# Performance work log

Measured on AMD Instinct MI355X. Metric: run time of the kernel, lower is better.

The kernel has to match this reference:

```python
import jax, jax.numpy as jnp
import numpy as np

DIM = 384
WIN = 16
NUM_HEADS = 12
HEAD_DIM = DIM // NUM_HEADS
SCALE = HEAD_DIM ** -0.5
EPS_NORM = 1e-12  # torch F.normalize eps


def setup_inputs() -> dict:
    key = jax.random.key(0)
    ks = jax.random.split(key, 5)
    B_ = 256
    x = jax.random.normal(ks[0], (B_, DIM, WIN, WIN), dtype=jnp.float32)
    qkv_w = jax.random.normal(ks[1], (3 * DIM, DIM), dtype=jnp.float32) * (DIM ** -0.5)
    qkv_b = jax.random.normal(ks[2], (3 * DIM,), dtype=jnp.float32) * 0.02
    proj_w = jax.random.normal(ks[3], (DIM, DIM), dtype=jnp.float32) * (DIM ** -0.5)
    proj_b = jax.random.normal(ks[4], (DIM,), dtype=jnp.float32) * 0.02
    return {"x": x, "qkv_w": qkv_w, "qkv_b": qkv_b, "proj_w": proj_w, "proj_b": proj_b}


def _l2norm(t):
    n = jnp.sqrt(jnp.sum(t * t, axis=-1, keepdims=True))
    return t / jnp.maximum(n, EPS_NORM)


def reference(x, qkv_w, qkv_b, proj_w, proj_b):
    B_, C, H, W = x.shape
    N = H * W
    xt = x.reshape(B_, C, N).transpose(0, 2, 1)  # (B_, N, C)
    qkv = jnp.einsum('bnc,oc->bno', xt, qkv_w) + qkv_b  # (B_, N, 3C)
    qkv = qkv.reshape(B_, N, 3, NUM_HEADS, HEAD_DIM).transpose(2, 0, 3, 1, 4)
    q, k, v = qkv[0], qkv[1], qkv[2]  # (B_, h, N, d)
    q = _l2norm(q)
    k = _l2norm(k)
    attn = jnp.einsum('bhnd,bhmd->bhnm', q, k) * SCALE
    attn = attn - jnp.max(attn, axis=-1, keepdims=True)
    attn = jax.nn.softmax(attn, axis=-1)
    attn = jnp.clip(attn, 1e-06, 1.0)
    out = jnp.einsum('bhnm,bhmd->bhnd', attn, v)  # (B_, h, N, d)
    out = out.transpose(0, 2, 1, 3).reshape(B_, N, C)
    out = jnp.einsum('bnc,oc->bno', out, proj_w) + proj_b
    return out.transpose(0, 2, 1).reshape(B_, C, H, W)
```

## Files before the change

### kernel.cpp

```cpp
#include <hip/hip_runtime.h>


#define DIM 384
#define NT 256
#define NH 12
#define HD 32
#define QSCALE (0.17677669529663687f * 1.4426950408889634f)

typedef __bf16 bf16;
typedef __bf16 bf16x4 __attribute__((ext_vector_type(4)));
typedef __bf16 bf16x8 __attribute__((ext_vector_type(8)));
typedef float f32x4 __attribute__((ext_vector_type(4)));
typedef int i32x2 __attribute__((ext_vector_type(2)));
typedef int i32x4 __attribute__((ext_vector_type(4)));

#define MFMA16(a, b, c) __builtin_amdgcn_mfma_f32_16x16x32_bf16(a, b, c, 0, 0, 0)

static __device__ __forceinline__ bf16x8 pack2(bf16x4 lo, bf16x4 hi) {
    i32x2 a = __builtin_bit_cast(i32x2, lo);
    i32x2 c = __builtin_bit_cast(i32x2, hi);
    i32x4 v = {a[0], a[1], c[0], c[1]};
    return __builtin_bit_cast(bf16x8, v);
}

__global__ void k_cast_w(const float* __restrict__ qkv_w, const float* __restrict__ proj_w,
                         bf16* __restrict__ wq, bf16* __restrict__ wp) {
    int i = blockIdx.x * 256 + threadIdx.x;
    if (i < 3 * DIM * DIM) wq[i] = (bf16)qkv_w[i];
    if (i < DIM * DIM)     wp[i] = (bf16)proj_w[i];
}

__global__ void k_transpose_cast(const float* __restrict__ x, bf16* __restrict__ xt) {
    __shared__ float tile[32][33];
    int b = blockIdx.z;
    int c0 = blockIdx.y * 32;
    int n0 = blockIdx.x * 32;
    int tx = threadIdx.x, ty = threadIdx.y;
    const float* xp = x + (size_t)b * DIM * NT;
#pragma unroll
    for (int i = 0; i < 4; ++i) {
        int c = c0 + ty + i * 8;
        tile[ty + i * 8][tx] = xp[(size_t)c * NT + n0 + tx];
    }
    __syncthreads();
    bf16* op = xt + (size_t)b * NT * DIM;
#pragma unroll
    for (int i = 0; i < 4; ++i) {
        int n = n0 + ty + i * 8;
        op[(size_t)n * DIM + c0 + tx] = (bf16)tile[tx][ty + i * 8];
    }
}

__launch_bounds__(512, 3)
__global__ void k_qkv_attn(const bf16* __restrict__ xt, const bf16* __restrict__ wq,
                           const float* __restrict__ qkv_b, bf16* __restrict__ attn_out) {
    __shared__ __align__(16) char smem[76800];
    bf16 (*wsm)[400] = (bf16(*)[400])smem;
    bf16 (*kn)[40]   = (bf16(*)[40])smem;
    bf16 (*vT)[264]  = (bf16(*)[264])(smem + 20480);
    bf16 (*qn)[32]   = (bf16(*)[32])(smem + 37376);
    __shared__ float bias_s[96];

    const int n_ = blockIdx.x;
    const int xcd = n_ & 7;
    const int ww = n_ >> 3;
    const int b = xcd * 32 + ww / 12;
    const int h = ww % 12;

    const int tid = threadIdx.x;
    const int lane = tid & 63, w = tid >> 6;
    const int l15 = lane & 15, quad = lane >> 4;

    if (tid < 96) {
        int which = tid >> 5;
        bias_s[tid] = qkv_b[which * DIM + h * HD + (tid & 31)];
    }
#pragma unroll
    for (int i = 0; i < 9; ++i) {
        int c = tid + i * 512;
        int row = c / 48, ch = c % 48;
        int grow = (row >> 5) * DIM + h * HD + (row & 31);
        *(bf16x8*)&wsm[row][ch * 8] = *(const bf16x8*)(wq + (size_t)grow * DIM + ch * 8);
    }
    __syncthreads();

    f32x4 acc[6][2];
#pragma unroll
    for (int jt = 0; jt < 6; ++jt)
#pragma unroll
        for (int tt = 0; tt < 2; ++tt) acc[jt][tt] = (f32x4){0.f, 0.f, 0.f, 0.f};

    const bf16* xrow[2];
#pragma unroll
    for (int tt = 0; tt < 2; ++tt) {
        int tok = w * 32 + tt * 16 + l15;
        xrow[tt] = xt + (size_t)(b * NT + tok) * DIM + quad * 8;
    }

    bf16x8 bx[2][2];
#pragma unroll
    for (int tt = 0; tt < 2; ++tt) bx[0][tt] = *(const bf16x8*)(xrow[tt]);

#pragma unroll
    for (int kc = 0; kc < 12; ++kc) {
        const int cur = kc & 1, nxt = cur ^ 1;
        if (kc < 11) {
            int k0 = (kc + 1) * 32;
#pragma unroll
            for (int tt = 0; tt < 2; ++tt) bx[nxt][tt] = *(const bf16x8*)(xrow[tt] + k0);
        }
        bf16x8 aw[6];
#pragma unroll
        for (int jt = 0; jt < 6; ++jt)
            aw[jt] = *(const bf16x8*)&wsm[jt * 16 + l15][kc * 32 + quad * 8];
#pragma unroll
        for (int jt = 0; jt < 6; ++jt)
#pragma unroll
            for (int tt = 0; tt < 2; ++tt)
                acc[jt][tt] = MFMA16(aw[jt], bx[cur][tt], acc[jt][tt]);
    }
    __syncthreads();

#pragma unroll
    for (int tt = 0; tt < 2; ++tt) {
        int tok = w * 32 + tt * 16 + l15;
        float sq = 0.f, sk = 0.f;
#pragma unroll
        for (int jt = 0; jt < 6; ++jt)
#pragma unroll
            for (int r = 0; r < 4; ++r) {
                int j = jt * 16 + quad * 4 + r;
                float t = acc[jt][tt][r] + bias_s[j];
                acc[jt][tt][r] = t;
                if (jt < 2) sq += t * t;
                else if (jt < 4) sk += t * t;
            }
        sq += __shfl_xor(sq, 16); sq += __shfl_xor(sq, 32);
        sk += __shfl_xor(sk, 16); sk += __shfl_xor(sk, 32);
        float iq = QSCALE / fmaxf(sqrtf(sq), 1e-12f);
        float ik = 1.f / fmaxf(sqrtf(sk), 1e-12f);

        bf16x4 q0v, q1v, k0v, k1v;
#pragma unroll
        for (int r = 0; r < 4; ++r) {
            q0v[r] = (bf16)(acc[0][tt][r] * iq);
            q1v[r] = (bf16)(acc[1][tt][r] * iq);
            k0v[r] = (bf16)(acc[2][tt][r] * ik);
            k1v[r] = (bf16)(acc[3][tt][r] * ik);
        }
        *(bf16x4*)&qn[tok][quad * 4]      = q0v;
        *(bf16x4*)&qn[tok][16 + quad * 4] = q1v;
        *(bf16x4*)&kn[tok][quad * 4]      = k0v;
        *(bf16x4*)&kn[tok][16 + quad * 4] = k1v;
#pragma unroll
        for (int r = 0; r < 4; ++r) {
            vT[quad * 4 + r][tok]      = (bf16)acc[4][tt][r];
            vT[16 + quad * 4 + r][tok] = (bf16)acc[5][tt][r];
        }
    }
    __syncthreads();

    bf16x8 qa[2];
#pragma unroll
    for (int qt = 0; qt < 2; ++qt)
        qa[qt] = *(const bf16x8*)&qn[w * 32 + qt * 16 + l15][quad * 8];

    const f32x4 zf = {0.f, 0.f, 0.f, 0.f};
    f32x4 o[2][2];
#pragma unroll
    for (int qt = 0; qt < 2; ++qt) { o[qt][0] = zf; o[qt][1] = zf; }
    float dsm[2] = {0.f, 0.f};

    bf16x8 kb0 = *(const bf16x8*)&kn[l15][quad * 8];
    bf16x8 kb1 = *(const bf16x8*)&kn[16 + l15][quad * 8];
    bf16x4 vp0 = *(const bf16x4*)&vT[l15][quad * 4];
    bf16x4 vp1 = *(const bf16x4*)&vT[l15][16 + quad * 4];
    bf16x4 vp2 = *(const bf16x4*)&vT[16 + l15][quad * 4];
    bf16x4 vp3 = *(const bf16x4*)&vT[16 + l15][16 + quad * 4];

#pragma unroll
    for (int kt = 0; kt < 8; ++kt) {
        f32x4 s00 = MFMA16(kb0, qa[0], zf);
        f32x4 s01 = MFMA16(kb1, qa[0], zf);
        f32x4 s10 = MFMA16(kb0, qa[1], zf);
        f32x4 s11 = MFMA16(kb1, qa[1], zf);
        bf16x8 vb0 = pack2(vp0, vp1);
        bf16x8 vb1 = pack2(vp2, vp3);
        if (kt < 7) {
            int nk = kt * 32 + 32;
            kb0 = *(const bf16x8*)&kn[nk + l15][quad * 8];
            kb1 = *(const bf16x8*)&kn[nk + 16 + l15][quad * 8];
            vp0 = *(const bf16x4*)&vT[l15][nk + quad * 4];
            vp1 = *(const bf16x4*)&vT[l15][nk + 16 + quad * 4];
            vp2 = *(const bf16x4*)&vT[16 + l15][nk + quad * 4];
            vp3 = *(const bf16x4*)&vT[16 + l15][nk + 16 + quad * 4];
        }
        bf16x8 pa0, pa1;
        float d0 = 0.f, d1 = 0.f;
#pragma unroll
        for (int r = 0; r < 4; ++r) {
            float p00 = __builtin_amdgcn_exp2f(s00[r]);
            float p01 = __builtin_amdgcn_exp2f(s01[r]);
            float p10 = __builtin_amdgcn_exp2f(s10[r]);
            float p11 = __builtin_amdgcn_exp2f(s11[r]);
            d0 += p00 + p01;  d1 += p10 + p11;
            pa0[r] = (bf16)p00; pa0[4 + r] = (bf16)p01;
            pa1[r] = (bf16)p10; pa1[4 + r] = (bf16)p11;
        }
        dsm[0] += d0;  dsm[1] += d1;
        o[0][0] = MFMA16(pa0, vb0, o[0][0]);
        o[0][1] = MFMA16(pa0, vb1, o[0][1]);
        o[1][0] = MFMA16(pa1, vb0, o[1][0]);
        o[1][1] = MFMA16(pa1, vb1, o[1][1]);
    }

#pragma unroll
    for (int qt = 0; qt < 2; ++qt) {
        dsm[qt] += __shfl_xor(dsm[qt], 16);
        dsm[qt] += __shfl_xor(dsm[qt], 32);
    }
    bf16* opbase = attn_out + (size_t)(b * NT + w * 32) * DIM + h * HD;
#pragma unroll
    for (int qt = 0; qt < 2; ++qt)
#pragma unroll
        for (int r = 0; r < 4; ++r) {
            float inv = 1.f / __shfl(dsm[qt], quad * 4 + r);
            int nq = qt * 16 + quad * 4 + r;
            opbase[(size_t)nq * DIM + l15]      = (bf16)(o[qt][0][r] * inv);
            opbase[(size_t)nq * DIM + 16 + l15] = (bf16)(o[qt][1][r] * inv);
        }
}

__launch_bounds__(256, 3)
__global__ void k_proj(const bf16* __restrict__ xa, const bf16* __restrict__ wp,
                       const float* __restrict__ proj_b, float* __restrict__ out) {
    __shared__ __align__(16) bf16 wsm[48][400];
    __shared__ float bias_s[48];
    const int n_ = blockIdx.x;
    const int xcd = n_ & 7;
    const int ww = n_ >> 3;
    const int b  = xcd * 32 + (ww >> 3);
    const int cb = ww & 7;

    const int tid = threadIdx.x;
    const int lane = tid & 63, w = tid >> 6;
    const int l15 = lane & 15, quad = lane >> 4;
    if (tid < 48) bias_s[tid] = proj_b[cb * 48 + tid];
#pragma unroll
    for (int i = 0; i < 9; ++i) {
        int c = tid + i * 256;
        int row = c / 48, ch = c % 48;
        *(bf16x8*)&wsm[row][ch * 8] =
            *(const bf16x8*)(wp + (size_t)(cb * 48 + row) * DIM + ch * 8);
    }
    __syncthreads();

    f32x4 acc[3][4];
#pragma unroll
    for (int jt = 0; jt < 3; ++jt)
#pragma unroll
        for (int tt = 0; tt < 4; ++tt) acc[jt][tt] = (f32x4){0.f, 0.f, 0.f, 0.f};

    const bf16* brow[4];
#pragma unroll
    for (int tt = 0; tt < 4; ++tt)
        brow[tt] = xa + (size_t)(b * NT + w * 64 + tt * 16 + l15) * DIM + quad * 8;

    bf16x8 bfr[2][4];
#pragma unroll
    for (int tt = 0; tt < 4; ++tt) bfr[0][tt] = *(const bf16x8*)(brow[tt]);

#pragma unroll
    for (int kc = 0; kc < 12; ++kc) {
        const int cur = kc & 1, nxt = cur ^ 1;
        if (kc < 11) {
            int k0 = (kc + 1) * 32;
#pragma unroll
            for (int tt = 0; tt < 4; ++tt) bfr[nxt][tt] = *(const bf16x8*)(brow[tt] + k0);
        }
        bf16x8 afr[3];
#pragma unroll
        for (int jt = 0; jt < 3; ++jt)
            afr[jt] = *(const bf16x8*)&wsm[jt * 16 + l15][kc * 32 + quad * 8];
#pragma unroll
        for (int jt = 0; jt < 3; ++jt)
#pragma unroll
            for (int tt = 0; tt < 4; ++tt)
                acc[jt][tt] = MFMA16(afr[jt], bfr[cur][tt], acc[jt][tt]);
    }

    float* op = out + (size_t)b * DIM * NT;
#pragma unroll
    for (int jt = 0; jt < 3; ++jt)
#pragma unroll
        for (int tt = 0; tt < 4; ++tt)
#pragma unroll
            for (int r = 0; r < 4; ++r) {
                int cl = jt * 16 + quad * 4 + r;
                int n  = w * 64 + tt * 16 + l15;
                op[(size_t)(cb * 48 + cl) * NT + n] = acc[jt][tt][r] + bias_s[cl];
            }
}

extern "C" void kernel_launch(void* const* d_in, const int* in_sizes, int n_in,
                              void* d_out, int out_size, void* d_ws, size_t ws_size,
                              hipStream_t stream) {
    const float* x      = (const float*)d_in[0];
    const float* qkv_w  = (const float*)d_in[1];
    const float* qkv_b  = (const float*)d_in[2];
    const float* proj_w = (const float*)d_in[3];
    const float* proj_b = (const float*)d_in[4];
    float* out = (float*)d_out;

    char* ws = (char*)d_ws;
    bf16* xt = (bf16*)ws;
    bf16* xa = (bf16*)(ws + 50331648);
    bf16* wq = (bf16*)(ws + 100663296);
    bf16* wp = (bf16*)(ws + 101548032);

    k_cast_w<<<dim3(1728), dim3(256), 0, stream>>>(qkv_w, proj_w, wq, wp);
    k_transpose_cast<<<dim3(8, 12, 256), dim3(32, 8), 0, stream>>>(x, xt);
    k_qkv_attn<<<dim3(NH * 256), dim3(512), 0, stream>>>(xt, wq, qkv_b, xa);
    k_proj<<<dim3(8 * 256), dim3(256), 0, stream>>>(xa, wp, proj_b, out);
}
```

Measured before the change: 367.7 us.

## Stage weights in K-halves to cut LDS and widen proj tiles

The QKV-attention kernel now stages its 96x384 weight slice into shared memory in two K-halves of 192 columns, with a barrier-separated reload between them. This shrinks its LDS footprint from about 75 KB to about 52 KB so more blocks can be resident per CU. The projection kernel now computes 96 output channels per block instead of 48, also staging weights in K-halves, which halves the grid and the number of times each activation row is re-read. The costs are extra barriers and an exposed weight reload mid-loop, plus doubled accumulator registers in k_proj with launch bounds lowered to 2 blocks per CU.

```diff
diff --git a/kernel.cpp b/kernel.cpp
--- a/kernel.cpp
+++ b/kernel.cpp
@@ -54,8 +54,8 @@
 __launch_bounds__(512, 3)
 __global__ void k_qkv_attn(const bf16* __restrict__ xt, const bf16* __restrict__ wq,
                            const float* __restrict__ qkv_b, bf16* __restrict__ attn_out) {
-    __shared__ __align__(16) char smem[76800];
-    bf16 (*wsm)[400] = (bf16(*)[400])smem;
+    __shared__ __align__(16) char smem[53760];
+    bf16 (*wsm)[200] = (bf16(*)[200])smem;
     bf16 (*kn)[40]   = (bf16(*)[40])smem;
     bf16 (*vT)[264]  = (bf16(*)[264])(smem + 20480);
     bf16 (*qn)[32]   = (bf16(*)[32])(smem + 37376);
@@ -75,13 +75,19 @@
         int which = tid >> 5;
         bias_s[tid] = qkv_b[which * DIM + h * HD + (tid & 31)];
     }
-#pragma unroll
-    for (int i = 0; i < 9; ++i) {
-        int c = tid + i * 512;
-        int row = c / 48, ch = c % 48;
-        int grow = (row >> 5) * DIM + h * HD + (row & 31);
-        *(bf16x8*)&wsm[row][ch * 8] = *(const bf16x8*)(wq + (size_t)grow * DIM + ch * 8);
-    }
+    auto stage_w = [&](int hk) {
+#pragma unroll
+        for (int i = 0; i < 5; ++i) {
+            int c = tid + i * 512;
+            if (c < 2304) {
+                int row = c / 24, ch = c % 24;
+                int grow = (row >> 5) * DIM + h * HD + (row & 31);
+                *(bf16x8*)&wsm[row][ch * 8] =
+                    *(const bf16x8*)(wq + (size_t)grow * DIM + hk * 192 + ch * 8);
+            }
+        }
+    };
+    stage_w(0);
     __syncthreads();
 
     f32x4 acc[6][2];
@@ -101,23 +107,32 @@
 #pragma unroll
     for (int tt = 0; tt < 2; ++tt) bx[0][tt] = *(const bf16x8*)(xrow[tt]);
 
-#pragma unroll
-    for (int kc = 0; kc < 12; ++kc) {
-        const int cur = kc & 1, nxt = cur ^ 1;
-        if (kc < 11) {
-            int k0 = (kc + 1) * 32;
-#pragma unroll
-            for (int tt = 0; tt < 2; ++tt) bx[nxt][tt] = *(const bf16x8*)(xrow[tt] + k0);
-        }
-        bf16x8 aw[6];
-#pragma unroll
-        for (int jt = 0; jt < 6; ++jt)
-            aw[jt] = *(const bf16x8*)&wsm[jt * 16 + l15][kc * 32 + quad * 8];
-#pragma unroll
-        for (int jt = 0; jt < 6; ++jt)
-#pragma unroll
-            for (int tt = 0; tt < 2; ++tt)
-                acc[jt][tt] = MFMA16(aw[jt], bx[cur][tt], acc[jt][tt]);
+#pragma unroll 1
+    for (int hk = 0; hk < 2; ++hk) {
+        if (hk) {
+            __syncthreads();
+            stage_w(1);
+            __syncthreads();
+        }
+#pragma unroll
+        for (int kc6 = 0; kc6 < 6; ++kc6) {
+            const int kc = hk * 6 + kc6;
+            const int cur = kc & 1, nxt = cur ^ 1;
+            if (kc < 11) {
+                int k0 = (kc + 1) * 32;
+#pragma unroll
+                for (int tt = 0; tt < 2; ++tt) bx[nxt][tt] = *(const bf16x8*)(xrow[tt] + k0);
+            }
+            bf16x8 aw[6];
+#pragma unroll
+            for (int jt = 0; jt < 6; ++jt)
+                aw[jt] = *(const bf16x8*)&wsm[jt * 16 + l15][kc6 * 32 + quad * 8];
+#pragma unroll
+            for (int jt = 0; jt < 6; ++jt)
+#pragma unroll
+                for (int tt = 0; tt < 2; ++tt)
+                    acc[jt][tt] = MFMA16(aw[jt], bx[cur][tt], acc[jt][tt]);
+        }
     }
     __syncthreads();
 
@@ -231,33 +246,37 @@
         }
 }
 
-__launch_bounds__(256, 3)
+__launch_bounds__(256, 2)
 __global__ void k_proj(const bf16* __restrict__ xa, const bf16* __restrict__ wp,
                        const float* __restrict__ proj_b, float* __restrict__ out) {
-    __shared__ __align__(16) bf16 wsm[48][400];
-    __shared__ float bias_s[48];
+    __shared__ __align__(16) bf16 wsm[96][200];
+    __shared__ float bias_s[96];
     const int n_ = blockIdx.x;
     const int xcd = n_ & 7;
     const int ww = n_ >> 3;
-    const int b  = xcd * 32 + (ww >> 3);
-    const int cb = ww & 7;
+    const int b  = xcd * 32 + (ww >> 2);
+    const int cb = ww & 3;
 
     const int tid = threadIdx.x;
     const int lane = tid & 63, w = tid >> 6;
     const int l15 = lane & 15, quad = lane >> 4;
-    if (tid < 48) bias_s[tid] = proj_b[cb * 48 + tid];
-#pragma unroll
-    for (int i = 0; i < 9; ++i) {
-        int c = tid + i * 256;
-        int row = c / 48, ch = c % 48;
-        *(bf16x8*)&wsm[row][ch * 8] =
-            *(const bf16x8*)(wp + (size_t)(cb * 48 + row) * DIM + ch * 8);
-    }
-    __syncthreads();
-
-    f32x4 acc[3][4];
-#pragma unroll
-    for (int jt = 0; jt < 3; ++jt)
+    if (tid < 96) bias_s[tid] = proj_b[cb * 96 + tid];
+
+    auto stage_w = [&](int hk) {
+#pragma unroll
+        for (int i = 0; i < 9; ++i) {
+            int c = tid + i * 256;
+            int row = c / 24, ch = c % 24;
+            *(bf16x8*)&wsm[row][ch * 8] =
+                *(const bf16x8*)(wp + (size_t)(cb * 96 + row) * DIM + hk * 192 + ch * 8);
+        }
+    };
+    stage_w(0);
+    __syncthreads();
+
+    f32x4 acc[6][4];
+#pragma unroll
+    for (int jt = 0; jt < 6; ++jt)
 #pragma unroll
         for (int tt = 0; tt < 4; ++tt) acc[jt][tt] = (f32x4){0.f, 0.f, 0.f, 0.f};
 
@@ -270,35 +289,44 @@
 #pragma unroll
     for (int tt = 0; tt < 4; ++tt) bfr[0][tt] = *(const bf16x8*)(brow[tt]);
 
-#pragma unroll
-    for (int kc = 0; kc < 12; ++kc) {
-        const int cur = kc & 1, nxt = cur ^ 1;
-        if (kc < 11) {
-            int k0 = (kc + 1) * 32;
-#pragma unroll
-            for (int tt = 0; tt < 4; ++tt) bfr[nxt][tt] = *(const bf16x8*)(brow[tt] + k0);
-        }
-        bf16x8 afr[3];
-#pragma unroll
-        for (int jt = 0; jt < 3; ++jt)
-            afr[jt] = *(const bf16x8*)&wsm[jt * 16 + l15][kc * 32 + quad * 8];
-#pragma unroll
-        for (int jt = 0; jt < 3; ++jt)
-#pragma unroll
-            for (int tt = 0; tt < 4; ++tt)
-                acc[jt][tt] = MFMA16(afr[jt], bfr[cur][tt], acc[jt][tt]);
+#pragma unroll 1
+    for (int hk = 0; hk < 2; ++hk) {
+        if (hk) {
+            __syncthreads();
+            stage_w(1);
+            __syncthreads();
+        }
+#pragma unroll
+        for (int kc6 = 0; kc6 < 6; ++kc6) {
+            const int kc = hk * 6 + kc6;
+            const int cur = kc & 1, nxt = cur ^ 1;
+            if (kc < 11) {
+                int k0 = (kc + 1) * 32;
+#pragma unroll
+                for (int tt = 0; tt < 4; ++tt) bfr[nxt][tt] = *(const bf16x8*)(brow[tt] + k0);
+            }
+            bf16x8 afr[6];
+#pragma unroll
+            for (int jt = 0; jt < 6; ++jt)
+                afr[jt] = *(const bf16x8*)&wsm[jt * 16 + l15][kc6 * 32 + quad * 8];
+#pragma unroll
+            for (int jt = 0; jt < 6; ++jt)
+#pragma unroll
+                for (int tt = 0; tt < 4; ++tt)
+                    acc[jt][tt] = MFMA16(afr[jt], bfr[cur][tt], acc[jt][tt]);
+        }
     }
 
     float* op = out + (size_t)b * DIM * NT;
 #pragma unroll
-    for (int jt = 0; jt < 3; ++jt)
+    for (int jt = 0; jt < 6; ++jt)
 #pragma unroll
         for (int tt = 0; tt < 4; ++tt)
 #pragma unroll
             for (int r = 0; r < 4; ++r) {
                 int cl = jt * 16 + quad * 4 + r;
                 int n  = w * 64 + tt * 16 + l15;
-                op[(size_t)(cb * 48 + cl) * NT + n] = acc[jt][tt][r] + bias_s[cl];
+                op[(size_t)(cb * 96 + cl) * NT + n] = acc[jt][tt][r] + bias_s[cl];
             }
 }
 
@@ -321,5 +349,5 @@
     k_cast_w<<<dim3(1728), dim3(256), 0, stream>>>(qkv_w, proj_w, wq, wp);
     k_transpose_cast<<<dim3(8, 12, 256), dim3(32, 8), 0, stream>>>(x, xt);
     k_qkv_attn<<<dim3(NH * 256), dim3(512), 0, stream>>>(xt, wq, qkv_b, xa);
-    k_proj<<<dim3(8 * 256), dim3(256), 0, stream>>>(xa, wp, proj_b, out);
-}
+    k_proj<<<dim3(4 * 256), dim3(256), 0, stream>>>(xa, wp, proj_b, out);
+}
```

New measurement: 372.9 us. About the same (+1.4%).
